# Kernel optimization log

Hardware: AMD Instinct MI355X
Metric: run time of the kernel (lower is better)

## Reference

```python
import jax, jax.numpy as jnp
import numpy as np

N = 50000      # nodes
E = 800000     # edges (before self loops)
NG = 512       # graphs in batch
D_IN = 128
D_H = 128
D_FC = 128
D_OUT = 2


def _gcn_conv(x, src, dst, norm, W, b, num_nodes):
    # x: [N, d_in] -> [N, d_out]; symmetric-normalized scatter-add over edges
    h = x @ W                              # [N, d_out]
    msg = h[src] * norm[:, None]           # [E+N, d_out]
    out = jax.ops.segment_sum(msg, dst, num_segments=num_nodes)
    return out + b


def setup_inputs() -> dict:
    key = jax.random.key(0)
    ks = jax.random.split(key, 12)
    x = jax.random.normal(ks[0], (N, D_IN), dtype=jnp.float32)
    edge_index = jax.random.randint(ks[1], (2, E), 0, N, dtype=jnp.int64)
    batch = jnp.sort(jax.random.randint(ks[2], (N,), 0, NG, dtype=jnp.int64))

    def glorot(k, shape):
        lim = float(np.sqrt(6.0 / (shape[0] + shape[1])))
        return jax.random.uniform(k, shape, jnp.float32, -lim, lim)

    return {
        "x": x, "edge_index": edge_index, "batch": batch,
        "W1": glorot(ks[3], (D_IN, D_H)), "b1": jnp.zeros((D_H,), jnp.float32),
        "W2": glorot(ks[4], (D_H, D_H)), "b2": jnp.zeros((D_H,), jnp.float32),
        "Wf1": glorot(ks[5], (D_H, D_FC)), "bf1": jnp.zeros((D_FC,), jnp.float32),
        "Wf2": glorot(ks[6], (D_FC, D_OUT)), "bf2": jnp.zeros((D_OUT,), jnp.float32),
    }


def reference(x, edge_index, batch, W1, b1, W2, b2, Wf1, bf1, Wf2, bf2):
    # add self loops (PyG GCNConv default)
    loops = jnp.arange(N, dtype=edge_index.dtype)
    src = jnp.concatenate([edge_index[0], loops])   # [E+N]
    dst = jnp.concatenate([edge_index[1], loops])   # [E+N]
    deg = jax.ops.segment_sum(jnp.ones_like(dst, dtype=x.dtype), dst, num_segments=N)
    dinv = jax.lax.rsqrt(deg)                       # deg >= 1 due to self loops
    norm = dinv[src] * dinv[dst]                    # [E+N]

    h = jax.nn.relu(_gcn_conv(x, src, dst, norm, W1, b1, N))
    h = jax.nn.relu(_gcn_conv(h, src, dst, norm, W2, b2, N))

    # global mean pool over graphs
    sums = jax.ops.segment_sum(h, batch, num_segments=NG)          # [NG, D_H]
    cnts = jax.ops.segment_sum(jnp.ones((N,), h.dtype), batch, num_segments=NG)
    g = sums / jnp.maximum(cnts, 1.0)[:, None]

    z = jax.nn.relu(g @ Wf1 + bf1)
    return z @ Wf2 + bf2
```

## Files before the change

kernel.cpp:

```cpp
#include <hip/hip_runtime.h>

typedef __attribute__((ext_vector_type(8))) short short8;
typedef __attribute__((ext_vector_type(4))) float f32x4;

__device__ __forceinline__ unsigned short f2b(float x) {
  unsigned u = __float_as_uint(x);
  u += 0x7FFF + ((u >> 16) & 1);
  return (unsigned short)(u >> 16);
}
__device__ __forceinline__ float b2f_lo(unsigned v) { return __uint_as_float(v << 16); }
__device__ __forceinline__ float b2f_hi(unsigned v) { return __uint_as_float(v & 0xFFFF0000u); }

#define EPB 4096
#define BKT 256
#define RPW 32

__global__ __launch_bounds__(256) void k_hist(const int* __restrict__ dst, int E,
                                              int nbuck, int* __restrict__ mat,
                                              int* __restrict__ tot) {
  __shared__ int h[256];
  int t = threadIdx.x;
  h[t] = 0;
  __syncthreads();
  int e0 = blockIdx.x * EPB, e1 = min(e0 + EPB, E);
  for (int e = e0 + t; e < e1; e += 256) atomicAdd(&h[dst[e] >> 8], 1);
  __syncthreads();
  if (t < nbuck) {
    mat[blockIdx.x * nbuck + t] = h[t];
    if (h[t]) atomicAdd(&tot[t], h[t]);
  }
}

__global__ __launch_bounds__(256) void k_excl(const int* __restrict__ tot, int nbuck,
                                              int* __restrict__ boff,
                                              int* __restrict__ rowptr, int N_) {
  __shared__ int s[256];
  int t = threadIdx.x;
  int v = (t < nbuck) ? tot[t] : 0;
  s[t] = v;
  __syncthreads();
  #pragma unroll
  for (int d = 1; d < 256; d <<= 1) {
    int u = (t >= d) ? s[t - d] : 0;
    __syncthreads();
    s[t] += u;
    __syncthreads();
  }
  if (t < nbuck) boff[t] = s[t] - v;
  if (t == 0) { boff[nbuck] = s[255]; rowptr[N_] = s[255]; }
}

__global__ __launch_bounds__(256) void k_colscan(int* __restrict__ mat, int neb, int nbuck,
                                                 const int* __restrict__ boff,
                                                 float* __restrict__ sums,
                                                 int* __restrict__ cnt, int ng) {
  __shared__ int s[256];
  int b = blockIdx.x, t = threadIdx.x;
  int v = (t < neb) ? mat[t * nbuck + b] : 0;
  s[t] = v;
  __syncthreads();
  #pragma unroll
  for (int d = 1; d < 256; d <<= 1) {
    int u = (t >= d) ? s[t - d] : 0;
    __syncthreads();
    s[t] += u;
    __syncthreads();
  }
  if (t < neb) mat[t * nbuck + b] = boff[b] + s[t] - v;
  int tot_e = ng * 128;
  for (int i = b * 256 + t; i < tot_e; i += gridDim.x * 256) sums[i] = 0.f;
  for (int i = b * 256 + t; i < ng; i += gridDim.x * 256) cnt[i] = 0;
}

__global__ __launch_bounds__(256) void k_part(const int* __restrict__ src,
                                              const int* __restrict__ dst, int E, int nbuck,
                                              const int* __restrict__ mat,
                                              unsigned* __restrict__ staged) {
  __shared__ int cur[256];
  int t = threadIdx.x;
  if (t < nbuck) cur[t] = mat[blockIdx.x * nbuck + t];
  __syncthreads();
  int e0 = blockIdx.x * EPB, e1 = min(e0 + EPB, E);
  for (int e = e0 + t; e < e1; e += 256) {
    int d = dst[e];
    int pos = atomicAdd(&cur[d >> 8], 1);
    staged[pos] = ((unsigned)(d & 255) << 16) | (unsigned)src[e];
  }
}

__global__ __launch_bounds__(256) void k_csr(const unsigned* __restrict__ staged,
                                             const int* __restrict__ boff, int N_,
                                             float* __restrict__ dinv, int* __restrict__ rowptr,
                                             unsigned short* __restrict__ csr16) {
  __shared__ int cnt[256];
  __shared__ int cur[256];
  int b = blockIdx.x, t = threadIdx.x;
  int lo = boff[b], hi = boff[b + 1];
  cnt[t] = 0;
  __syncthreads();
  for (int i = lo + t; i < hi; i += 256) atomicAdd(&cnt[staged[i] >> 16], 1);
  __syncthreads();
  int v = cnt[t];
  #pragma unroll
  for (int d = 1; d < 256; d <<= 1) {
    int u = (t >= d) ? cnt[t - d] : 0;
    __syncthreads();
    cnt[t] += u;
    __syncthreads();
  }
  int start = lo + cnt[t] - v;
  cur[t] = start;
  int node = (b << 8) + t;
  if (node < N_) {
    rowptr[node] = start;
    dinv[node] = rsqrtf((float)(v + 1));
  }
  __syncthreads();
  for (int i = lo + t; i < hi; i += 256) {
    unsigned e = staged[i];
    int pos = atomicAdd(&cur[e >> 16], 1);
    csr16[pos] = (unsigned short)(e & 0xFFFFu);
  }
}

__global__ __launch_bounds__(256) void k_prepW(const float* __restrict__ W,
                                               unsigned short* __restrict__ Wt,
                                               int* __restrict__ tot_zero) {
  __shared__ float t[32][33];
  int tx = threadIdx.x & 31, ty = threadIdx.x >> 5;
  int bx = blockIdx.x & 3, by = blockIdx.x >> 2;
  if (tot_zero && blockIdx.x == 0) tot_zero[threadIdx.x] = 0;
  #pragma unroll
  for (int i = 0; i < 4; ++i)
    t[ty + i * 8][tx] = W[(by * 32 + ty + i * 8) * 128 + bx * 32 + tx];
  __syncthreads();
  #pragma unroll
  for (int i = 0; i < 4; ++i)
    Wt[(bx * 32 + ty + i * 8) * 128 + by * 32 + tx] = f2b(t[tx][ty + i * 8]);
}

template<int A_F32>
__global__ __launch_bounds__(256) void k_mfma_gemm(
    const void* __restrict__ Ap, const unsigned short* __restrict__ Wt,
    const float* __restrict__ dinv, unsigned short* __restrict__ Out, int M)
{
  int wv = threadIdx.x >> 6, lane = threadIdx.x & 63;
  int r0 = blockIdx.x * 64 + wv * 16;
  if (r0 >= M) return;
  int arow = r0 + (lane & 15);
  int kb = (lane >> 4) * 8;
  short8 a[4];
  if (A_F32) {
    const float* Ar = (const float*)Ap + (size_t)arow * 128 + kb;
    #pragma unroll
    for (int ks = 0; ks < 4; ++ks) {
      float4 u = *(const float4*)(Ar + ks * 32);
      float4 v = *(const float4*)(Ar + ks * 32 + 4);
      short8 tt;
      tt[0] = (short)f2b(u.x); tt[1] = (short)f2b(u.y);
      tt[2] = (short)f2b(u.z); tt[3] = (short)f2b(u.w);
      tt[4] = (short)f2b(v.x); tt[5] = (short)f2b(v.y);
      tt[6] = (short)f2b(v.z); tt[7] = (short)f2b(v.w);
      a[ks] = tt;
    }
  } else {
    const unsigned short* Ar = (const unsigned short*)Ap + (size_t)arow * 128 + kb;
    #pragma unroll
    for (int ks = 0; ks < 4; ++ks)
      a[ks] = *(const short8*)(Ar + ks * 32);
  }
  f32x4 acc[8];
  #pragma unroll
  for (int i = 0; i < 8; ++i) acc[i] = (f32x4){0.f, 0.f, 0.f, 0.f};
  const unsigned short* Bc = Wt + (size_t)(lane & 15) * 128 + kb;
  #pragma unroll
  for (int ct = 0; ct < 8; ++ct) {
    const unsigned short* B = Bc + ct * 16 * 128;
    #pragma unroll
    for (int ks = 0; ks < 4; ++ks)
      acc[ct] = __builtin_amdgcn_mfma_f32_16x16x32_bf16(
          a[ks], *(const short8*)(B + ks * 32), acc[ct], 0, 0, 0);
  }
  int orow = r0 + (lane >> 4) * 4;
  int ocol = lane & 15;
  float s0 = dinv[orow], s1 = dinv[orow + 1], s2 = dinv[orow + 2], s3 = dinv[orow + 3];
  #pragma unroll
  for (int ct = 0; ct < 8; ++ct) {
    unsigned short* o = Out + (size_t)orow * 128 + ct * 16 + ocol;
    o[0]   = f2b(acc[ct][0] * s0);
    o[128] = f2b(acc[ct][1] * s1);
    o[256] = f2b(acc[ct][2] * s2);
    o[384] = f2b(acc[ct][3] * s3);
  }
}

__global__ __launch_bounds__(256) void k_gather_post(
    const unsigned short* __restrict__ csr16, const int* __restrict__ rowptr,
    const unsigned short* __restrict__ P, const float* __restrict__ dinv,
    const float* __restrict__ bias, unsigned short* __restrict__ R, int n)
{
  int node = blockIdx.x * 4 + (threadIdx.x >> 6);
  if (node >= n) return;
  int lane = threadIdx.x & 63;
  int lo = rowptr[node], hi = rowptr[node + 1];
  float ax = 0.f, ay = 0.f;
  #pragma unroll 4
  for (int e = lo; e < hi; ++e) {
    unsigned s = csr16[e];
    unsigned v = ((const unsigned*)(P + (size_t)s * 128))[lane];
    ax += b2f_lo(v); ay += b2f_hi(v);
  }
  float dv = dinv[node];
  unsigned hv = ((const unsigned*)(P + (size_t)node * 128))[lane];
  float2 b = ((const float2*)bias)[lane];
  float rx = fmaxf(dv * (ax + b2f_lo(hv)) + b.x, 0.f);
  float ry = fmaxf(dv * (ay + b2f_hi(hv)) + b.y, 0.f);
  unsigned pack = (unsigned)f2b(rx) | ((unsigned)f2b(ry) << 16);
  ((unsigned*)(R + (size_t)node * 128))[lane] = pack;
}

__global__ __launch_bounds__(256) void k_pool_sum(
    const unsigned short* __restrict__ h2, const int* __restrict__ batch, int n,
    float* __restrict__ sums, int* __restrict__ cnt)
{
  int wid = blockIdx.x * 4 + (threadIdx.x >> 6);
  int lane = threadIdx.x & 63;
  int r0 = wid * RPW;
  if (r0 >= n) return;
  int r1 = min(r0 + RPW, n);
  const unsigned* H = (const unsigned*)h2;
  int gcur = batch[r0];
  float ax = 0.f, ay = 0.f;
  int run = 0;
  for (int r = r0; r < r1; ++r) {
    int g = batch[r];
    if (g != gcur) {
      atomicAdd(&sums[(size_t)gcur * 128 + 2 * lane], ax);
      atomicAdd(&sums[(size_t)gcur * 128 + 2 * lane + 1], ay);
      if (lane == 0) atomicAdd(&cnt[gcur], run);
      ax = ay = 0.f; run = 0; gcur = g;
    }
    unsigned v = H[(size_t)r * 64 + lane];
    ax += b2f_lo(v); ay += b2f_hi(v); ++run;
  }
  atomicAdd(&sums[(size_t)gcur * 128 + 2 * lane], ax);
  atomicAdd(&sums[(size_t)gcur * 128 + 2 * lane + 1], ay);
  if (lane == 0) atomicAdd(&cnt[gcur], run);
}

__global__ __launch_bounds__(128) void k_fc(
    const float* __restrict__ sums, const int* __restrict__ cnt,
    const float* __restrict__ Wf1, const float* __restrict__ bf1,
    const float* __restrict__ Wf2, const float* __restrict__ bf2,
    float* __restrict__ out)
{
  __shared__ float gl[128];
  __shared__ float red0[128];
  __shared__ float red1[128];
  int g = blockIdx.x, t = threadIdx.x;
  float c = (float)cnt[g];
  gl[t] = sums[(size_t)g * 128 + t] / fmaxf(c, 1.f);
  __syncthreads();
  float z0 = 0.f, z1 = 0.f, z2 = 0.f, z3 = 0.f;
  #pragma unroll
  for (int k = 0; k < 32; ++k) {
    z0 += gl[k]      * Wf1[k * 128 + t];
    z1 += gl[k + 32] * Wf1[(k + 32) * 128 + t];
    z2 += gl[k + 64] * Wf1[(k + 64) * 128 + t];
    z3 += gl[k + 96] * Wf1[(k + 96) * 128 + t];
  }
  float z = fmaxf((z0 + z1) + (z2 + z3) + bf1[t], 0.f);
  red0[t] = z * Wf2[2 * t];
  red1[t] = z * Wf2[2 * t + 1];
  __syncthreads();
  #pragma unroll
  for (int d = 64; d > 0; d >>= 1) {
    if (t < d) { red0[t] += red0[t + d]; red1[t] += red1[t + d]; }
    __syncthreads();
  }
  if (t == 0) {
    out[g * 2]     = red0[0] + bf2[0];
    out[g * 2 + 1] = red1[0] + bf2[1];
  }
}

extern "C" void kernel_launch(void* const* d_in, const int* in_sizes, int n_in,
                              void* d_out, int out_size, void* d_ws, size_t ws_size,
                              hipStream_t stream) {
  const float* x    = (const float*)d_in[0];
  const int*   ei   = (const int*)d_in[1];
  const int*   batch= (const int*)d_in[2];
  const float* W1   = (const float*)d_in[3];
  const float* b1   = (const float*)d_in[4];
  const float* W2   = (const float*)d_in[5];
  const float* b2   = (const float*)d_in[6];
  const float* Wf1  = (const float*)d_in[7];
  const float* bf1  = (const float*)d_in[8];
  const float* Wf2  = (const float*)d_in[9];
  const float* bf2  = (const float*)d_in[10];
  float* out = (float*)d_out;

  const int N  = in_sizes[0] / 128;
  const int E  = in_sizes[1] / 2;
  const int NG = out_size / 2;
  const int* srcp = ei;
  const int* dstp = ei + E;

  const int nbuck = (N + BKT - 1) / BKT;
  const int neb   = (E + EPB - 1) / EPB;

  char* ws = (char*)d_ws;
  size_t off = 0;
  auto carve = [&](size_t bytes) { void* p = ws + off; off += (bytes + 255) & ~(size_t)255; return p; };
  float* dinv   = (float*)carve((size_t)N * 4);
  int*   rowptr = (int*)  carve((size_t)(N + 1) * 4);
  int*   boff   = (int*)  carve((size_t)(nbuck + 1) * 4);
  int*   tot    = (int*)  carve((size_t)256 * 4);
  int*   mat    = (int*)  carve((size_t)neb * nbuck * 4);
  unsigned*       staged = (unsigned*)      carve((size_t)E * 4);
  unsigned short* csr16  = (unsigned short*)carve((size_t)E * 2);
  unsigned short* Wt1 = (unsigned short*)carve(128 * 128 * 2);
  unsigned short* Wt2 = (unsigned short*)carve(128 * 128 * 2);
  float* sums   = (float*)carve((size_t)NG * 128 * 4);
  int*   cntg   = (int*)  carve((size_t)NG * 4);
  const size_t nb_row = (size_t)N * 128 * 2;
  unsigned short* U0 = (unsigned short*)carve(nb_row);
  unsigned short* U1 = (unsigned short*)carve(nb_row);

  k_prepW<<<16, 256, 0, stream>>>(W1, Wt1, tot);
  k_prepW<<<16, 256, 0, stream>>>(W2, Wt2, nullptr);

  k_hist   <<<neb, 256, 0, stream>>>(dstp, E, nbuck, mat, tot);
  k_excl   <<<1, 256, 0, stream>>>(tot, nbuck, boff, rowptr, N);
  k_colscan<<<nbuck, 256, 0, stream>>>(mat, neb, nbuck, boff, sums, cntg, NG);
  k_part   <<<neb, 256, 0, stream>>>(srcp, dstp, E, nbuck, mat, staged);
  k_csr    <<<nbuck, 256, 0, stream>>>(staged, boff, N, dinv, rowptr, csr16);

  const int gblocks = (N + 63) / 64;
  k_mfma_gemm<1><<<gblocks, 256, 0, stream>>>(x, Wt1, dinv, U0, N);
  k_gather_post<<<(N + 3) / 4, 256, 0, stream>>>(csr16, rowptr, U0, dinv, b1, U1, N);
  k_mfma_gemm<0><<<gblocks, 256, 0, stream>>>(U1, Wt2, dinv, U0, N);
  k_gather_post<<<(N + 3) / 4, 256, 0, stream>>>(csr16, rowptr, U0, dinv, b2, U1, N);

  const int pblocks = (N + RPW * 4 - 1) / (RPW * 4);
  k_pool_sum<<<pblocks, 256, 0, stream>>>(U1, batch, N, sums, cntg);
  k_fc<<<NG, 128, 0, stream>>>(sums, cntg, Wf1, bf1, Wf2, bf2, out);
}
```

Measured before the change: 190.0 us.

## Fuse setup kernels and widen gather to half-wave per node with 4-edge batching

Merges the two weight-transpose launches with the destination histogram into one kernel. The bucket totals are now computed redundantly in each offsets block instead of through a global atomic plus a separate single-block scan, which cuts the preprocessing chain from seven launches to four. The gather kernel now assigns 32 lanes per node with 8-byte loads and processes four edges per iteration, giving more memory-level parallelism and twice as many nodes per block. The cost is that every offsets block rereads the whole count matrix column-wise, and an extra buffer holds the scanned offsets.

Measured after the change: 213.1 us. 1.12x slower.

```diff
diff --git a/kernel.cpp b/kernel.cpp
--- a/kernel.cpp
+++ b/kernel.cpp
@@ -15,29 +15,49 @@
 #define BKT 256
 #define RPW 32
 
-__global__ __launch_bounds__(256) void k_hist(const int* __restrict__ dst, int E,
-                                              int nbuck, int* __restrict__ mat,
-                                              int* __restrict__ tot) {
+__global__ __launch_bounds__(256) void k_setup(
+    const float* __restrict__ W1, unsigned short* __restrict__ Wt1,
+    const float* __restrict__ W2, unsigned short* __restrict__ Wt2,
+    const int* __restrict__ dst, int E, int nbuck, int* __restrict__ mat)
+{
+  __shared__ float tile[32][33];
   __shared__ int h[256];
   int t = threadIdx.x;
-  h[t] = 0;
-  __syncthreads();
-  int e0 = blockIdx.x * EPB, e1 = min(e0 + EPB, E);
-  for (int e = e0 + t; e < e1; e += 256) atomicAdd(&h[dst[e] >> 8], 1);
-  __syncthreads();
-  if (t < nbuck) {
-    mat[blockIdx.x * nbuck + t] = h[t];
-    if (h[t]) atomicAdd(&tot[t], h[t]);
-  }
-}
-
-__global__ __launch_bounds__(256) void k_excl(const int* __restrict__ tot, int nbuck,
-                                              int* __restrict__ boff,
-                                              int* __restrict__ rowptr, int N_) {
+  if (blockIdx.x < 32) {
+    const float* W = (blockIdx.x < 16) ? W1 : W2;
+    unsigned short* Wt = (blockIdx.x < 16) ? Wt1 : Wt2;
+    int bid = blockIdx.x & 15;
+    int tx = t & 31, ty = t >> 5;
+    int bx = bid & 3, by = bid >> 2;
+    #pragma unroll
+    for (int i = 0; i < 4; ++i)
+      tile[ty + i * 8][tx] = W[(by * 32 + ty + i * 8) * 128 + bx * 32 + tx];
+    __syncthreads();
+    #pragma unroll
+    for (int i = 0; i < 4; ++i)
+      Wt[(bx * 32 + ty + i * 8) * 128 + by * 32 + tx] = f2b(tile[tx][ty + i * 8]);
+  } else {
+    int blk = blockIdx.x - 32;
+    h[t] = 0;
+    __syncthreads();
+    int e0 = blk * EPB, e1 = min(e0 + EPB, E);
+    for (int e = e0 + t; e < e1; e += 256) atomicAdd(&h[dst[e] >> 8], 1);
+    __syncthreads();
+    if (t < nbuck) mat[blk * nbuck + t] = h[t];
+  }
+}
+
+__global__ __launch_bounds__(256) void k_offsets(
+    const int* __restrict__ mat, int* __restrict__ matB, int neb, int nbuck,
+    int* __restrict__ boff, int* __restrict__ rowptr, int N_,
+    float* __restrict__ sums, int* __restrict__ cnt, int ng)
+{
   __shared__ int s[256];
-  int t = threadIdx.x;
-  int v = (t < nbuck) ? tot[t] : 0;
-  s[t] = v;
+  int b = blockIdx.x, t = threadIdx.x;
+  int tsum = 0;
+  if (t < nbuck)
+    for (int r = 0; r < neb; ++r) tsum += mat[r * nbuck + t];
+  s[t] = tsum;
   __syncthreads();
   #pragma unroll
   for (int d = 1; d < 256; d <<= 1) {
@@ -46,16 +66,14 @@
     s[t] += u;
     __syncthreads();
   }
-  if (t < nbuck) boff[t] = s[t] - v;
-  if (t == 0) { boff[nbuck] = s[255]; rowptr[N_] = s[255]; }
-}
-
-__global__ __launch_bounds__(256) void k_colscan(int* __restrict__ mat, int neb, int nbuck,
-                                                 const int* __restrict__ boff,
-                                                 float* __restrict__ sums,
-                                                 int* __restrict__ cnt, int ng) {
-  __shared__ int s[256];
-  int b = blockIdx.x, t = threadIdx.x;
+  int excl = s[t] - tsum;
+  if (t == b && t < nbuck) boff[b] = excl;
+  if (b == 0 && t == 0) { boff[nbuck] = s[255]; rowptr[N_] = s[255]; }
+  __syncthreads();
+  s[t] = excl;
+  __syncthreads();
+  int base = s[b];
+  __syncthreads();
   int v = (t < neb) ? mat[t * nbuck + b] : 0;
   s[t] = v;
   __syncthreads();
@@ -66,7 +84,7 @@
     s[t] += u;
     __syncthreads();
   }
-  if (t < neb) mat[t * nbuck + b] = boff[b] + s[t] - v;
+  if (t < neb) matB[t * nbuck + b] = base + s[t] - v;
   int tot_e = ng * 128;
   for (int i = b * 256 + t; i < tot_e; i += gridDim.x * 256) sums[i] = 0.f;
   for (int i = b * 256 + t; i < ng; i += gridDim.x * 256) cnt[i] = 0;
@@ -74,11 +92,11 @@
 
 __global__ __launch_bounds__(256) void k_part(const int* __restrict__ src,
                                               const int* __restrict__ dst, int E, int nbuck,
-                                              const int* __restrict__ mat,
+                                              const int* __restrict__ matB,
                                               unsigned* __restrict__ staged) {
   __shared__ int cur[256];
   int t = threadIdx.x;
-  if (t < nbuck) cur[t] = mat[blockIdx.x * nbuck + t];
+  if (t < nbuck) cur[t] = matB[blockIdx.x * nbuck + t];
   __syncthreads();
   int e0 = blockIdx.x * EPB, e1 = min(e0 + EPB, E);
   for (int e = e0 + t; e < e1; e += 256) {
@@ -121,22 +139,6 @@
     int pos = atomicAdd(&cur[e >> 16], 1);
     csr16[pos] = (unsigned short)(e & 0xFFFFu);
   }
-}
-
-__global__ __launch_bounds__(256) void k_prepW(const float* __restrict__ W,
-                                               unsigned short* __restrict__ Wt,
-                                               int* __restrict__ tot_zero) {
-  __shared__ float t[32][33];
-  int tx = threadIdx.x & 31, ty = threadIdx.x >> 5;
-  int bx = blockIdx.x & 3, by = blockIdx.x >> 2;
-  if (tot_zero && blockIdx.x == 0) tot_zero[threadIdx.x] = 0;
-  #pragma unroll
-  for (int i = 0; i < 4; ++i)
-    t[ty + i * 8][tx] = W[(by * 32 + ty + i * 8) * 128 + bx * 32 + tx];
-  __syncthreads();
-  #pragma unroll
-  for (int i = 0; i < 4; ++i)
-    Wt[(bx * 32 + ty + i * 8) * 128 + by * 32 + tx] = f2b(t[tx][ty + i * 8]);
 }
 
 template<int A_F32>
@@ -199,24 +201,40 @@
     const unsigned short* __restrict__ P, const float* __restrict__ dinv,
     const float* __restrict__ bias, unsigned short* __restrict__ R, int n)
 {
-  int node = blockIdx.x * 4 + (threadIdx.x >> 6);
+  int node = blockIdx.x * 8 + (threadIdx.x >> 5);
   if (node >= n) return;
-  int lane = threadIdx.x & 63;
+  int lane = threadIdx.x & 31;
   int lo = rowptr[node], hi = rowptr[node + 1];
-  float ax = 0.f, ay = 0.f;
-  #pragma unroll 4
-  for (int e = lo; e < hi; ++e) {
-    unsigned s = csr16[e];
-    unsigned v = ((const unsigned*)(P + (size_t)s * 128))[lane];
-    ax += b2f_lo(v); ay += b2f_hi(v);
+  float a0 = 0.f, a1 = 0.f, a2 = 0.f, a3 = 0.f;
+  int e = lo;
+  for (; e + 4 <= hi; e += 4) {
+    int s0 = csr16[e], s1 = csr16[e + 1], s2 = csr16[e + 2], s3 = csr16[e + 3];
+    uint2 v0 = ((const uint2*)(P + (size_t)s0 * 128))[lane];
+    uint2 v1 = ((const uint2*)(P + (size_t)s1 * 128))[lane];
+    uint2 v2 = ((const uint2*)(P + (size_t)s2 * 128))[lane];
+    uint2 v3 = ((const uint2*)(P + (size_t)s3 * 128))[lane];
+    a0 += b2f_lo(v0.x) + b2f_lo(v1.x) + b2f_lo(v2.x) + b2f_lo(v3.x);
+    a1 += b2f_hi(v0.x) + b2f_hi(v1.x) + b2f_hi(v2.x) + b2f_hi(v3.x);
+    a2 += b2f_lo(v0.y) + b2f_lo(v1.y) + b2f_lo(v2.y) + b2f_lo(v3.y);
+    a3 += b2f_hi(v0.y) + b2f_hi(v1.y) + b2f_hi(v2.y) + b2f_hi(v3.y);
+  }
+  for (; e < hi; ++e) {
+    int s = csr16[e];
+    uint2 v = ((const uint2*)(P + (size_t)s * 128))[lane];
+    a0 += b2f_lo(v.x); a1 += b2f_hi(v.x);
+    a2 += b2f_lo(v.y); a3 += b2f_hi(v.y);
   }
   float dv = dinv[node];
-  unsigned hv = ((const unsigned*)(P + (size_t)node * 128))[lane];
-  float2 b = ((const float2*)bias)[lane];
-  float rx = fmaxf(dv * (ax + b2f_lo(hv)) + b.x, 0.f);
-  float ry = fmaxf(dv * (ay + b2f_hi(hv)) + b.y, 0.f);
-  unsigned pack = (unsigned)f2b(rx) | ((unsigned)f2b(ry) << 16);
-  ((unsigned*)(R + (size_t)node * 128))[lane] = pack;
+  uint2 hv = ((const uint2*)(P + (size_t)node * 128))[lane];
+  float4 bb = ((const float4*)bias)[lane];
+  float r0 = fmaxf(dv * (a0 + b2f_lo(hv.x)) + bb.x, 0.f);
+  float r1 = fmaxf(dv * (a1 + b2f_hi(hv.x)) + bb.y, 0.f);
+  float r2 = fmaxf(dv * (a2 + b2f_lo(hv.y)) + bb.z, 0.f);
+  float r3 = fmaxf(dv * (a3 + b2f_hi(hv.y)) + bb.w, 0.f);
+  uint2 pack;
+  pack.x = (unsigned)f2b(r0) | ((unsigned)f2b(r1) << 16);
+  pack.y = (unsigned)f2b(r2) | ((unsigned)f2b(r3) << 16);
+  ((uint2*)(R + (size_t)node * 128))[lane] = pack;
 }
 
 __global__ __launch_bounds__(256) void k_pool_sum(
@@ -315,8 +333,8 @@
   float* dinv   = (float*)carve((size_t)N * 4);
   int*   rowptr = (int*)  carve((size_t)(N + 1) * 4);
   int*   boff   = (int*)  carve((size_t)(nbuck + 1) * 4);
-  int*   tot    = (int*)  carve((size_t)256 * 4);
   int*   mat    = (int*)  carve((size_t)neb * nbuck * 4);
+  int*   matB   = (int*)  carve((size_t)neb * nbuck * 4);
   unsigned*       staged = (unsigned*)      carve((size_t)E * 4);
   unsigned short* csr16  = (unsigned short*)carve((size_t)E * 2);
   unsigned short* Wt1 = (unsigned short*)carve(128 * 128 * 2);
@@ -327,20 +345,16 @@
   unsigned short* U0 = (unsigned short*)carve(nb_row);
   unsigned short* U1 = (unsigned short*)carve(nb_row);
 
-  k_prepW<<<16, 256, 0, stream>>>(W1, Wt1, tot);
-  k_prepW<<<16, 256, 0, stream>>>(W2, Wt2, nullptr);
-
-  k_hist   <<<neb, 256, 0, stream>>>(dstp, E, nbuck, mat, tot);
-  k_excl   <<<1, 256, 0, stream>>>(tot, nbuck, boff, rowptr, N);
-  k_colscan<<<nbuck, 256, 0, stream>>>(mat, neb, nbuck, boff, sums, cntg, NG);
-  k_part   <<<neb, 256, 0, stream>>>(srcp, dstp, E, nbuck, mat, staged);
-  k_csr    <<<nbuck, 256, 0, stream>>>(staged, boff, N, dinv, rowptr, csr16);
+  k_setup<<<32 + neb, 256, 0, stream>>>(W1, Wt1, W2, Wt2, dstp, E, nbuck, mat);
+  k_offsets<<<nbuck, 256, 0, stream>>>(mat, matB, neb, nbuck, boff, rowptr, N, sums, cntg, NG);
+  k_part<<<neb, 256, 0, stream>>>(srcp, dstp, E, nbuck, matB, staged);
+  k_csr <<<nbuck, 256, 0, stream>>>(staged, boff, N, dinv, rowptr, csr16);
 
   const int gblocks = (N + 63) / 64;
   k_mfma_gemm<1><<<gblocks, 256, 0, stream>>>(x, Wt1, dinv, U0, N);
-  k_gather_post<<<(N + 3) / 4, 256, 0, stream>>>(csr16, rowptr, U0, dinv, b1, U1, N);
+  k_gather_post<<<(N + 7) / 8, 256, 0, stream>>>(csr16, rowptr, U0, dinv, b1, U1, N);
   k_mfma_gemm<0><<<gblocks, 256, 0, stream>>>(U1, Wt2, dinv, U0, N);
-  k_gather_post<<<(N + 3) / 4, 256, 0, stream>>>(csr16, rowptr, U0, dinv, b2, U1, N);
+  k_gather_post<<<(N + 7) / 8, 256, 0, stream>>>(csr16, rowptr, U0, dinv, b2, U1, N);
 
   const int pblocks = (N + RPW * 4 - 1) / (RPW * 4);
   k_pool_sum<<<pblocks, 256, 0, stream>>>(U1, batch, N, sums, cntg);
```
